# Optimization experiments

Measured on AMD Instinct MI355X. Metric: run time of the kernel, lower is better.

The kernel has to match this reference:

```python
import jax, jax.numpy as jnp
import numpy as np

N = 10000            # nodes
E = 320000           # edges (avg degree 32)
L = 4                # layers
S = 64               # hidden 0e multiplicity
V = 16               # hidden 1o multiplicity
EMB = 32             # node-attr embedding dim
NB = 8               # bessel basis per channel (r and v -> 2*NB edge feats)
MR = 2.5             # max_radius
DEG = 32.0           # num_neighbors
GS = S + V           # gate input scalars: 64 scalars + 16 gates
NW = S * 2 + V * 2 + V * 2   # 192 per-edge tensor-product weights
MAXT = 100           # max atom types


def _semi_unitary(K):
    # Newton-Schulz orthogonalization: K^T K -> I (semi-unitary uplift matrix)
    K = K / jnp.linalg.norm(K)
    for _ in range(10):
        K = 1.5 * K - 0.5 * K @ (K.T @ K)
    return K


def _smooth_cutoff(t):
    u = 2.0 * (t - 1.0)
    y = (1.0 - jnp.cos(jnp.pi * u)) * 0.5
    return jnp.where(u > 0, 0.0, jnp.where(u < -1.0, 1.0, y))


def _edge_geom(d):
    # d: (E,3) edge vector. Returns cutoff-weighted 1x1o SH (component norm) and bessel features.
    r = jnp.linalg.norm(d, axis=1)                       # (E,)
    sh = np.sqrt(3.0) * d / r[:, None]                   # spherical harmonics 1x1o
    attr = _smooth_cutoff(r / MR)[:, None] * sh          # (E,3)
    k = jnp.arange(1, NB + 1, dtype=jnp.float32) * jnp.pi
    feat = np.sqrt(2.0 / MR) * jnp.sin(k * (r / MR)[:, None]) / r[:, None]
    return attr, feat * np.sqrt(NB)                      # (E,3), (E,NB)


def _fctp(s, v, attr, Ws, Wv):
    # FullyConnectedTensorProduct with pure-scalar (0e) node attr == attr-weighted per-irrep linear
    os = jnp.einsum('ni,ne,oie->no', s, attr, Ws) / np.sqrt(s.shape[1] * EMB)
    ov = jnp.einsum('nim,ne,oie->nom', v, attr, Wv) / np.sqrt(v.shape[1] * EMB)
    return os, ov


def _forward(x, node_attr, edge_src, edge_dst, emb_table, PU_K, h, mix,
             si_Ws, si_Wv, sc_Ws, sc_Wv, lin1_Ws, lin1_Wv, lin2_Ws, lin2_Wv,
             fc_W1, fc_b1, fc_W2, fc_b2, fc_W3, fc_b3):
    attr = emb_table[node_attr]                          # (N,EMB)
    K = _semi_unitary(PU_K)                              # (V,2)
    yv = jnp.einsum('ui,nim->num', K, x.reshape(N, 2, 3))  # uplift vectors
    ys = jnp.zeros((N, S), x.dtype)
    ys_old, yv_old = ys, yv
    c_s, c_x = np.sin(np.pi / 8), np.cos(np.pi / 8)
    for i in range(L):
        ar, fr = _edge_geom(x[:, :3][edge_src] - x[:, :3][edge_dst])
        av, fv = _edge_geom(x[:, 3:][edge_src] - x[:, 3:][edge_dst])
        a = jnp.stack([ar, av], axis=1)                  # (E,2,3) = 2x1o edge attr
        ef = jnp.concatenate([fr, fv], axis=1)           # (E,2*NB)
        # radial MLP -> per-edge TP weights
        hd = jax.nn.silu(ef @ fc_W1[i] + fc_b1[i])
        hd = jax.nn.silu(hd @ fc_W2[i] + fc_b2[i])
        w = hd @ fc_W3[i] + fc_b3[i]                     # (E,NW)
        w1 = w[:, :S * 2].reshape(-1, S, 2)
        w2 = w[:, S * 2:S * 2 + V * 2].reshape(-1, V, 2)
        w3 = w[:, S * 2 + V * 2:].reshape(-1, V, 2)
        # conv: lin1 -> gather -> TP -> scatter -> lin2 ; plus self-connection
        fs, fvv = _fctp(ys, yv, attr, lin1_Ws[i], lin1_Wv[i])
        s_src, v_src = fs[edge_src], fvv[edge_src]
        # 0e x 1o -> 1o (uvu)
        o1 = jnp.einsum('euv,eu,evm->eum', w1, s_src, a) / np.sqrt(2.0)   # (E,S,3)
        # 1o x 1o -> 0e (uvu)
        dots = jnp.einsum('eum,evm->euv', v_src, a)
        o2 = jnp.einsum('euv,euv->eu', w2, dots) / np.sqrt(6.0)           # (E,V)
        # 1o x 1o -> 1o (cross, uvu)
        cr = jnp.cross(v_src[:, :, None, :], a[:, None, :, :])            # (E,V,2,3)
        o3 = jnp.einsum('euv,euvm->eum', w3, cr) / 2.0                    # (E,V,3)
        mid_s = jax.ops.segment_sum(o2, edge_dst, num_segments=N) / np.sqrt(DEG)
        mid_v = jax.ops.segment_sum(jnp.concatenate([o1, o3], axis=1), edge_dst,
                                    num_segments=N) / np.sqrt(DEG)        # (N,S+V,3)
        cs2, cv2 = _fctp(mid_s, mid_v, attr, lin2_Ws[i], lin2_Wv[i])      # (N,GS),(N,V,3)
        scs, scv = _fctp(ys, yv, attr, sc_Ws[i], sc_Wv[i])
        conv_s = c_s * scs + c_x * cs2
        conv_v = c_s * scv + c_x * cv2
        # gate: silu scalars, sigmoid gates * gated vectors
        gns = jax.nn.silu(conv_s[:, :S])
        gnv = jax.nn.sigmoid(conv_s[:, S:])[:, :, None] * conv_v
        # self-interaction: per-irrep linear
        sis = ys @ si_Ws[i].T / np.sqrt(S)
        siv = jnp.einsum('oi,nim->nom', si_Wv[i], yv) / np.sqrt(V)
        # leapfrog update
        h2 = h[i] ** 2
        ns = 2.0 * ys - ys_old + h2 * (mix[i] * gns + (mix[i] - 1.0) * sis)
        nv = 2.0 * yv - yv_old + h2 * (mix[i] * gnv + (mix[i] - 1.0) * siv)
        ys_old, yv_old = ys, yv
        ys, yv = ns, nv
        x = jnp.einsum('ui,num->nim', K, yv).reshape(N, 6)   # project
    return x


def setup_inputs() -> dict:
    key = jax.random.key(0)
    ks = jax.random.split(key, 24)
    def g(i, sh, fan=1.0):
        return jax.random.normal(ks[i], sh, dtype=jnp.float32) / np.sqrt(fan)
    edge_src = jax.random.randint(ks[20], (E,), 0, N, dtype=jnp.int32)
    off = jax.random.randint(ks[21], (E,), 1, N, dtype=jnp.int32)
    edge_dst = (edge_src + off) % N                      # guarantees src != dst
    return {
        'x': g(0, (N, 6)),
        'batch': jnp.zeros((N,), jnp.int32),
        'node_attr': jax.random.randint(ks[22], (N,), 0, MAXT, dtype=jnp.int32),
        'edge_src': edge_src,
        'edge_dst': edge_dst,
        'emb_table': g(1, (MAXT, EMB)),
        'PU_K': g(2, (V, 2)),
        'h': jnp.full((L,), 0.01, jnp.float32),
        'mix': jnp.full((L,), 0.5, jnp.float32),
        'si_Ws': g(3, (L, S, S)), 'si_Wv': g(4, (L, V, V)),
        'sc_Ws': g(5, (L, GS, S, EMB)), 'sc_Wv': g(6, (L, V, V, EMB)),
        'lin1_Ws': g(7, (L, S, S, EMB)), 'lin1_Wv': g(8, (L, V, V, EMB)),
        'lin2_Ws': g(9, (L, GS, V, EMB)), 'lin2_Wv': g(10, (L, V, S + V, EMB)),
        'fc_W1': g(11, (L, 2 * NB, 64), 2 * NB), 'fc_b1': jnp.zeros((L, 64), jnp.float32),
        'fc_W2': g(12, (L, 64, 64), 64), 'fc_b2': jnp.zeros((L, 64), jnp.float32),
        'fc_W3': g(13, (L, 64, NW), 64), 'fc_b3': jnp.zeros((L, NW), jnp.float32),
    }


def reference(x, batch, node_attr, edge_src, edge_dst, emb_table, PU_K, h, mix,
              si_Ws, si_Wv, sc_Ws, sc_Wv, lin1_Ws, lin1_Wv, lin2_Ws, lin2_Wv,
              fc_W1, fc_b1, fc_W2, fc_b2, fc_W3, fc_b3):
    return _forward(x, node_attr, edge_src, edge_dst, emb_table, PU_K, h, mix,
                    si_Ws, si_Wv, sc_Ws, sc_Wv, lin1_Ws, lin1_Wv, lin2_Ws, lin2_Wv,
                    fc_W1, fc_b1, fc_W2, fc_b2, fc_W3, fc_b3)
```

## Files before the change

### kernel.cpp

```cpp
#include <hip/hip_runtime.h>
#include <hip/hip_fp8.h>
#include <math.h>

#define NN 10000
#define NE 320000
#define PI_F 3.14159265358979323846f

typedef __attribute__((ext_vector_type(8))) short short8x;
typedef __attribute__((ext_vector_type(4))) float float4x;

#if defined(__has_builtin)
#if __has_builtin(__builtin_amdgcn_cvt_pk_fp8_f32) && __has_builtin(__builtin_amdgcn_cvt_f32_fp8)
#define HW_FP8 1
#endif
#endif

__device__ __forceinline__ unsigned short f2b(float f) {
    unsigned b = __float_as_uint(f);
    return (unsigned short)((b + 0x7FFFu + ((b >> 16) & 1u)) >> 16);
}
__device__ __forceinline__ float b2f(unsigned short u) {
    return __uint_as_float(((unsigned)u) << 16);
}
__device__ __forceinline__ float silu(float x) {
    return x / (1.f + __expf(-x));
}
__device__ __forceinline__ unsigned char f2e4(float f) {
#ifdef HW_FP8
    int r = __builtin_amdgcn_cvt_pk_fp8_f32(f, f, 0, false);
    return (unsigned char)(r & 0xff);
#else
    __hip_fp8_e4m3 q(f);
    return (unsigned char)q.__x;
#endif
}
__device__ __forceinline__ float e42f(unsigned char v) {
#ifdef HW_FP8
    return __builtin_amdgcn_cvt_f32_fp8((int)v, 0);
#else
    __hip_fp8_e4m3 q;
    q.__x = (__hip_fp8_storage_t)v;
    return (float)q;
#endif
}
__device__ __forceinline__ float e4sel(unsigned word, int sel) {
#ifdef HW_FP8
    switch (sel & 3) {
        case 0:  return __builtin_amdgcn_cvt_f32_fp8((int)word, 0);
        case 1:  return __builtin_amdgcn_cvt_f32_fp8((int)word, 1);
        case 2:  return __builtin_amdgcn_cvt_f32_fp8((int)word, 2);
        default: return __builtin_amdgcn_cvt_f32_fp8((int)word, 3);
    }
#else
    return e42f((unsigned char)((word >> (8*(sel & 3))) & 0xffu));
#endif
}
__device__ __forceinline__ unsigned pk4(float a, float b, float c, float d) {
#ifdef HW_FP8
    unsigned w = (unsigned)__builtin_amdgcn_cvt_pk_fp8_f32(a, b, 0, false);
    w = (unsigned)__builtin_amdgcn_cvt_pk_fp8_f32(c, d, (int)w, true);
    return w;
#else
    return (unsigned)f2e4(a) | ((unsigned)f2e4(b) << 8) |
           ((unsigned)f2e4(c) << 16) | ((unsigned)f2e4(d) << 24);
#endif
}

__global__ void k_newton_kernel(const float* __restrict__ PU, float* __restrict__ Kout)
{
    if (threadIdx.x != 0 || blockIdx.x != 0) return;
    float K[32];
    float nrm = 0.f;
    for (int i = 0; i < 32; ++i) { K[i] = PU[i]; nrm += K[i]*K[i]; }
    float inv = 1.0f / sqrtf(nrm);
    for (int i = 0; i < 32; ++i) K[i] *= inv;
    for (int it = 0; it < 10; ++it) {
        float m00 = 0.f, m01 = 0.f, m11 = 0.f;
        for (int u = 0; u < 16; ++u) {
            float a = K[2*u], b = K[2*u+1];
            m00 += a*a; m01 += a*b; m11 += b*b;
        }
        for (int u = 0; u < 16; ++u) {
            float a = K[2*u], b = K[2*u+1];
            K[2*u]   = 1.5f*a - 0.5f*(a*m00 + b*m01);
            K[2*u+1] = 1.5f*b - 0.5f*(a*m01 + b*m11);
        }
    }
    for (int i = 0; i < 32; ++i) Kout[i] = K[i];
}

__global__ __launch_bounds__(256) void init_all_kernel(
    const float* __restrict__ x, const float* __restrict__ K,
    float* __restrict__ xp, float* __restrict__ yv0, float* __restrict__ yv1,
    float* __restrict__ ys0, float* __restrict__ ys1, float* __restrict__ fsb,
    float* __restrict__ midb)
{
    int tid = blockIdx.x*256 + threadIdx.x;
    if (tid < NN*8) {
        int n = tid >> 3, c = tid & 7;
        xp[tid] = (c < 6) ? x[n*6 + c] : 0.f;
        return;
    }
    int t2 = tid - NN*8;
    if (t2 < NN*48) {
        int n = t2/48, j = t2%48, u = j/3, m = j%3;
        float v = K[2*u]*x[n*6+m] + K[2*u+1]*x[n*6+3+m];
        yv0[t2] = v; yv1[t2] = v;
        return;
    }
    t2 -= NN*48;
    if (t2 < NN*64) { ys0[t2] = 0.f; ys1[t2] = 0.f; fsb[t2] = 0.f; return; }
    t2 -= NN*64;
    if (t2 < NN*256) midb[t2] = 0.f;
}

__global__ void init_fvv_kernel(const float* __restrict__ yv, const int* __restrict__ types,
                                const float* __restrict__ lin1vT0, float* __restrict__ fvv)
{
    int tid = blockIdx.x*blockDim.x + threadIdx.x;
    if (tid >= NN*48) return;
    int n = tid/48, j = tid%48, o = j/3, m = j%3;
    int t = types[n];
    const float* W = lin1vT0 + (size_t)t*256;
    float acc = 0.f;
    #pragma unroll
    for (int i = 0; i < 16; ++i) acc += yv[n*48 + i*3 + m]*W[i*16 + o];
    fvv[tid] = acc;
}

__device__ __forceinline__ void be_body(const float* __restrict__ W, const float* __restrict__ emb,
                                        float* __restrict__ out, int id, int O, int I, float scale)
{
    int o = id % O; int r = id / O;
    int i = r % I; r /= I;
    int t = r % 100; int l = r / 100;
    const float* w  = W + (((size_t)l*O + o)*I + i)*32;
    const float* em = emb + (size_t)t*32;
    float acc = 0.f;
    #pragma unroll
    for (int e = 0; e < 32; ++e) acc += w[e]*em[e];
    out[id] = acc*scale;
}

#define PREP_TOTAL (2048000 + 1638400 + 512000 + 512000 + 102400 + 102400 + 49152 + 16384 + 16384 + 8192 + 1024)
__global__ __launch_bounds__(256) void prep_kernel(
    const float* __restrict__ lin1_Ws, const float* __restrict__ lin1_Wv,
    const float* __restrict__ sc_Ws,   const float* __restrict__ sc_Wv,
    const float* __restrict__ lin2_Ws, const float* __restrict__ lin2_Wv,
    const float* __restrict__ si_Ws,   const float* __restrict__ si_Wv,
    const float* __restrict__ fc_W1,   const float* __restrict__ fc_W2,
    const float* __restrict__ fc_W3,   const float* __restrict__ emb,
    float* __restrict__ lin1sT, float* __restrict__ lin1vT,
    float* __restrict__ scsT,   float* __restrict__ scvT,
    float* __restrict__ lin2sT, float* __restrict__ lin2vT,
    float* __restrict__ siWsT,  float* __restrict__ siWvT,
    unsigned short* __restrict__ w1bp, unsigned short* __restrict__ w2bp,
    unsigned short* __restrict__ w3bf)
{
    const float s2048 = 0.022097086912079608f;
    const float s512  = 0.044194173824159216f;
    const float s2560 = 0.019764235376052372f;
    int tid = blockIdx.x*256 + threadIdx.x;
    if (tid < 2048000) { be_body(sc_Ws,   emb, scsT,   tid, 80, 64, s2048); return; }
    tid -= 2048000;
    if (tid < 1638400) { be_body(lin1_Ws, emb, lin1sT, tid, 64, 64, s2048); return; }
    tid -= 1638400;
    if (tid < 512000)  { be_body(lin2_Ws, emb, lin2sT, tid, 80, 16, s512);  return; }
    tid -= 512000;
    if (tid < 512000)  { be_body(lin2_Wv, emb, lin2vT, tid, 16, 80, s2560); return; }
    tid -= 512000;
    if (tid < 102400)  { be_body(lin1_Wv, emb, lin1vT, tid, 16, 16, s512);  return; }
    tid -= 102400;
    if (tid < 102400)  { be_body(sc_Wv,   emb, scvT,   tid, 16, 16, s512);  return; }
    tid -= 102400;
    if (tid < 49152) {
        int o = tid % 64; int r = tid / 64; int i = r % 192; int l = r / 192;
        w3bf[tid] = f2b(fc_W3[((size_t)l*64 + o)*192 + i]);
        return;
    }
    tid -= 49152;
    if (tid < 16384) {
        int o = tid % 64; int r = tid / 64; int i = r % 64; int l = r / 64;
        siWsT[tid] = si_Ws[((size_t)l*64 + o)*64 + i]*0.125f;
        return;
    }
    tid -= 16384;
    if (tid < 16384) {
        int kk = tid % 64; int r = tid / 64; int n = r % 64; int l = r / 64;
        w2bp[tid] = f2b(fc_W2[((size_t)l*64 + kk)*64 + n]);
        return;
    }
    tid -= 16384;
    if (tid < 8192) {
        int kk = tid % 32; int r = tid / 32; int n = r % 64; int l = r / 64;
        float v = (kk < 16) ? fc_W1[((size_t)l*16 + kk)*64 + n] : 0.f;
        w1bp[tid] = f2b(v);
        return;
    }
    tid -= 8192;
    if (tid < 1024) {
        int o = tid % 16; int r = tid / 16; int i = r % 16; int l = r / 16;
        siWvT[tid] = si_Wv[((size_t)l*16 + o)*16 + i]*0.25f;
    }
}

__global__ void hist_kernel(const int* __restrict__ dst, int* __restrict__ deg)
{
    int e = blockIdx.x*256 + threadIdx.x;
    if (e < NE) atomicAdd(&deg[dst[e]], 1);
}

__global__ __launch_bounds__(256) void scan_kernel(const int* __restrict__ deg,
                                                   int* __restrict__ segoff,
                                                   int* __restrict__ cursor)
{
    __shared__ int part[256];
    int tid = threadIdx.x;
    int base = tid*40;
    int s = 0;
    for (int i = 0; i < 40; ++i) { int idx = base+i; if (idx < NN) s += deg[idx]; }
    part[tid] = s;
    __syncthreads();
    for (int o = 1; o < 256; o <<= 1) {
        int v = (tid >= o) ? part[tid-o] : 0;
        __syncthreads();
        part[tid] += v;
        __syncthreads();
    }
    int excl = part[tid] - s;
    for (int i = 0; i < 40; ++i) {
        int idx = base+i;
        if (idx < NN) { segoff[idx] = excl; cursor[idx] = excl; excl += deg[idx]; }
        else if (idx == NN) { segoff[NN] = excl; }
    }
}

__global__ void scatter_kernel(const int* __restrict__ src, const int* __restrict__ dst,
                               int* __restrict__ cursor,
                               int* __restrict__ srcs, int* __restrict__ dsts)
{
    int e = blockIdx.x*256 + threadIdx.x;
    if (e >= NE) return;
    int d = dst[e];
    int p = atomicAdd(&cursor[d], 1);
    srcs[p] = src[e]; dsts[p] = d;
}

__global__ __launch_bounds__(256, 6) void edge_fused_kernel(
    const float* __restrict__ xp,
    const int* __restrict__ srcs, const int* __restrict__ dsts,
    const unsigned short* __restrict__ w1b,
    const float* __restrict__ b1,
    const unsigned short* __restrict__ w2b,
    const float* __restrict__ b2,
    const unsigned short* __restrict__ w3b,
    const float* __restrict__ b3,
    const float* __restrict__ fs, const float* __restrict__ fvv,
    float* __restrict__ mid)
{
    __shared__ __align__(16) unsigned char smem[192*68];
    __shared__ float abuf[6][68];
    __shared__ int ssrc[64], sdst[64];
    __shared__ unsigned smaskl[2];
    unsigned short* hbuf = (unsigned short*)smem;
    int lane = threadIdx.x & 63;
    int wid  = threadIdx.x >> 6;
    int eblk = blockIdx.x * 64;
    int row16 = lane & 15, quad = lane >> 4;
    int erow = 16*wid + row16;

    if (threadIdx.x < 64) {
        int tid = threadIdx.x;
        int own = dsts[eblk + tid];
        ssrc[tid] = srcs[eblk + tid];
        int pidx = eblk + tid - ((tid > 0) ? 1 : 0);
        int prev = dsts[pidx];
        sdst[tid] = own;
        bool nb = (tid > 0) && (own != prev);
        unsigned long long bm = __ballot(nb);
        if (tid == 0) { smaskl[0] = (unsigned)bm; smaskl[1] = (unsigned)(bm >> 32); }
    }

    if (lane < 32) {
        int eidx = 16*wid + (lane & 15);
        int half = lane >> 4;
        int p = eblk + eidx;
        int s = srcs[p], d = dsts[p];
        int off = 3*half;
        const float* xs = xp + (size_t)s*8 + off;
        const float* xd = xp + (size_t)d*8 + off;
        float d0 = xs[0]-xd[0], d1 = xs[1]-xd[1], d2 = xs[2]-xd[2];
        float r = sqrtf(d0*d0 + d1*d1 + d2*d2);
        float invr = 1.0f/r;
        float u = 0.8f*r - 2.0f;
        float cut = (u > 0.f) ? 0.f : ((u < -1.f) ? 1.f : 0.5f*(1.f - __cosf(PI_F*u)));
        float sc = 1.7320508075688772f*cut*invr;
        abuf[off+0][eidx] = sc*d0;
        abuf[off+1][eidx] = sc*d1;
        abuf[off+2][eidx] = sc*d2;
        float fsc = 2.5298221281347035f*invr;
        float wr = 1.2566370614359172f*r;
        unsigned epk[4];
        #pragma unroll
        for (int k = 0; k < 4; ++k) {
            float e0 = fsc*__sinf((float)(2*k+1)*wr);
            float e1 = fsc*__sinf((float)(2*k+2)*wr);
            epk[k] = (unsigned)f2b(e0) | ((unsigned)f2b(e1) << 16);
        }
        uint4* hr = (uint4*)(hbuf + eidx*72);
        uint4 q; q.x = epk[0]; q.y = epk[1]; q.z = epk[2]; q.w = epk[3];
        hr[half] = q;
        uint4 qz; qz.x = 0; qz.y = 0; qz.z = 0; qz.w = 0;
        hr[2+half] = qz;
    }

    {
        short8x a = *(const short8x*)(hbuf + erow*72 + quad*8);
        float4x c[4];
        #pragma unroll
        for (int nt = 0; nt < 4; ++nt) {
            short8x b = *(const short8x*)(w1b + ((size_t)(nt*16 + row16))*32 + quad*8);
            c[nt] = __builtin_amdgcn_mfma_f32_16x16x32_bf16(a, b, (float4x){0.f,0.f,0.f,0.f}, 0, 0, 0);
        }
        #pragma unroll
        for (int nt = 0; nt < 4; ++nt) {
            float bias = b1[nt*16 + row16];
            #pragma unroll
            for (int r = 0; r < 4; ++r) {
                float h = silu(c[nt][r] + bias);
                hbuf[(16*wid + quad*4 + r)*72 + nt*16 + row16] = f2b(h);
            }
        }
    }
    {
        short8x a0v = *(const short8x*)(hbuf + erow*72 + 0*32 + quad*8);
        short8x a1v = *(const short8x*)(hbuf + erow*72 + 1*32 + quad*8);
        float4x c[4];
        #pragma unroll
        for (int nt = 0; nt < 4; ++nt) {
            short8x b0 = *(const short8x*)(w2b + ((size_t)(nt*16 + row16))*64 + 0*32 + quad*8);
            float4x t = __builtin_amdgcn_mfma_f32_16x16x32_bf16(a0v, b0, (float4x){0.f,0.f,0.f,0.f}, 0, 0, 0);
            short8x b1v = *(const short8x*)(w2b + ((size_t)(nt*16 + row16))*64 + 1*32 + quad*8);
            c[nt] = __builtin_amdgcn_mfma_f32_16x16x32_bf16(a1v, b1v, t, 0, 0, 0);
        }
        #pragma unroll
        for (int nt = 0; nt < 4; ++nt) {
            float bias = b2[nt*16 + row16];
            #pragma unroll
            for (int r = 0; r < 4; ++r) {
                float h = silu(c[nt][r] + bias);
                hbuf[(16*wid + quad*4 + r)*72 + nt*16 + row16] = f2b(h);
            }
        }
    }
    {
        short8x a0v = *(const short8x*)(hbuf + erow*72 + 0*32 + quad*8);
        short8x a1v = *(const short8x*)(hbuf + erow*72 + 1*32 + quad*8);
        __syncthreads();
        float4x acc[12];
        #pragma unroll
        for (int nt = 0; nt < 12; ++nt) {
            short8x b0 = *(const short8x*)(w3b + ((size_t)(nt*16 + row16))*64 + 0*32 + quad*8);
            float4x t = __builtin_amdgcn_mfma_f32_16x16x32_bf16(a0v, b0, (float4x){0.f,0.f,0.f,0.f}, 0, 0, 0);
            short8x b1v = *(const short8x*)(w3b + ((size_t)(nt*16 + row16))*64 + 1*32 + quad*8);
            acc[nt] = __builtin_amdgcn_mfma_f32_16x16x32_bf16(a1v, b1v, t, 0, 0, 0);
        }
        #pragma unroll
        for (int nt = 0; nt < 12; ++nt) {
            unsigned pw = pk4(acc[nt][0], acc[nt][1], acc[nt][2], acc[nt][3]);
            *(unsigned*)(smem + (size_t)(nt*16 + row16)*68 + 16*wid + quad*4) = pw;
        }
    }
    __syncthreads();

    {
        unsigned mk0 = __builtin_amdgcn_readfirstlane(smaskl[0]);
        unsigned mk1 = __builtin_amdgcn_readfirstlane(smaskl[1]);
        bool iso1 = (wid < 2);
        int h = iso1 ? wid : (wid - 2);
        unsigned mkh = (h ? mk1 : mk0) & ~1u;
        int ebase = 32*h;
        int dcur = sdst[ebase];

        if (iso1) {
            const unsigned char* wp = smem + (size_t)(2*lane)*68;
            float bA = b3[2*lane], bB = b3[2*lane+1];
            float acc0 = 0.f, acc1 = 0.f, acc2 = 0.f;
            #pragma unroll
            for (int ch = 0; ch < 8; ++ch) {
                int e4 = ebase + 4*ch;
                int4 sv = *(const int4*)&ssrc[e4];
                float f0 = fs[(size_t)sv.x*64 + lane];
                float f1 = fs[(size_t)sv.y*64 + lane];
                float f2 = fs[(size_t)sv.z*64 + lane];
                float f3 = fs[(size_t)sv.w*64 + lane];
                unsigned wa4 = *(const unsigned*)(wp + e4);
                unsigned wb4 = *(const unsigned*)(wp + 68 + e4);
                float4x a00 = *(const float4x*)(&abuf[0][e4]);
                float4x a01 = *(const float4x*)(&abuf[1][e4]);
                float4x a02 = *(const float4x*)(&abuf[2][e4]);
                float4x a10 = *(const float4x*)(&abuf[3][e4]);
                float4x a11 = *(const float4x*)(&abuf[4][e4]);
                float4x a12 = *(const float4x*)(&abuf[5][e4]);
                float fv[4] = {f0, f1, f2, f3};
                float q0[4], q1[4], q2[4];
                #pragma unroll
                for (int k = 0; k < 4; ++k) {
                    float f = fv[k];
                    float wa = (e4sel(wa4, k) + bA)*f;
                    float wb = (e4sel(wb4, k) + bB)*f;
                    q0[k] = wa*a00[k] + wb*a10[k];
                    q1[k] = wa*a01[k] + wb*a11[k];
                    q2[k] = wa*a02[k] + wb*a12[k];
                }
                unsigned mch = (mkh >> (4*ch)) & 15u;
                if (mch == 0) {
                    acc0 += (q0[0] + q0[1]) + (q0[2] + q0[3]);
                    acc1 += (q1[0] + q1[1]) + (q1[2] + q1[3]);
                    acc2 += (q2[0] + q2[1]) + (q2[2] + q2[3]);
                } else {
                    #pragma unroll
                    for (int k = 0; k < 4; ++k) {
                        if (mch & (1u << k)) {
                            float* mrow = mid + (size_t)dcur*256;
                            atomicAdd(mrow + 3*lane + 0, acc0*0.125f);
                            atomicAdd(mrow + 3*lane + 1, acc1*0.125f);
                            atomicAdd(mrow + 3*lane + 2, acc2*0.125f);
                            acc0 = acc1 = acc2 = 0.f;
                            dcur = sdst[e4 + k];
                        }
                        acc0 += q0[k]; acc1 += q1[k]; acc2 += q2[k];
                    }
                }
            }
            float* mrow = mid + (size_t)dcur*256;
            atomicAdd(mrow + 3*lane + 0, acc0*0.125f);
            atomicAdd(mrow + 3*lane + 1, acc1*0.125f);
            atomicAdd(mrow + 3*lane + 2, acc2*0.125f);
        } else {
            bool iso2 = lane < 16;
            int j3 = lane - 16;
            int u3 = j3 / 3;
            int m3 = j3 - 3*u3;
            int m1 = (m3 == 2) ? 0 : (m3 + 1);
            int m2 = 3 - m3 - m1;
            const unsigned char* wp;
            int rA, rB, rC;
            const float* aX0; const float* aY0; const float* aZ0;
            const float* aX1; const float* aY1; const float* aZ1;
            float bA, bB, sgn, gam, FS;
            if (iso2) {
                wp = smem + (size_t)(128 + 2*lane)*68;
                bA = b3[128 + 2*lane]; bB = b3[129 + 2*lane];
                rA = 3*lane; rB = 3*lane + 1; rC = 3*lane + 2;
                aX0 = &abuf[0][0]; aY0 = &abuf[1][0]; aZ0 = &abuf[2][0];
                aX1 = &abuf[3][0]; aY1 = &abuf[4][0]; aZ1 = &abuf[5][0];
                sgn = 1.f; gam = 1.f; FS = 0.07216878364870323f;
            } else {
                wp = smem + (size_t)(160 + 2*u3)*68;
                bA = b3[160 + 2*u3]; bB = b3[161 + 2*u3];
                rA = 3*u3 + m1; rB = 3*u3 + m2; rC = 0;
                aX0 = &abuf[m2][0]; aY0 = &abuf[m1][0]; aZ0 = &abuf[0][0];
                aX1 = &abuf[3+m2][0]; aY1 = &abuf[3+m1][0]; aZ1 = &abuf[3][0];
                sgn = -1.f; gam = 0.f; FS = 0.08838834764831845f;
            }
            int cb = 192 + lane;
            float accb = 0.f;
            #pragma unroll
            for (int ch = 0; ch < 8; ++ch) {
                int e4 = ebase + 4*ch;
                int4 sv = *(const int4*)&ssrc[e4];
                float fa0 = fvv[(size_t)sv.x*48 + rA];
                float fb0 = fvv[(size_t)sv.x*48 + rB];
                float fc0 = fvv[(size_t)sv.x*48 + rC];
                float fa1 = fvv[(size_t)sv.y*48 + rA];
                float fb1 = fvv[(size_t)sv.y*48 + rB];
                float fc1 = fvv[(size_t)sv.y*48 + rC];
                float fa2 = fvv[(size_t)sv.z*48 + rA];
                float fb2 = fvv[(size_t)sv.z*48 + rB];
                float fc2 = fvv[(size_t)sv.z*48 + rC];
                float fa3 = fvv[(size_t)sv.w*48 + rA];
                float fb3 = fvv[(size_t)sv.w*48 + rB];
                float fc3 = fvv[(size_t)sv.w*48 + rC];
                unsigned wa4 = *(const unsigned*)(wp + e4);
                unsigned wb4 = *(const unsigned*)(wp + 68 + e4);
                float4x x0 = *(const float4x*)(aX0 + e4);
                float4x y0 = *(const float4x*)(aY0 + e4);
                float4x z0 = *(const float4x*)(aZ0 + e4);
                float4x x1 = *(const float4x*)(aX1 + e4);
                float4x y1 = *(const float4x*)(aY1 + e4);
                float4x z1 = *(const float4x*)(aZ1 + e4);
                float fav[4] = {fa0, fa1, fa2, fa3};
                float fbv[4] = {fb0, fb1, fb2, fb3};
                float fcv[4] = {fc0, fc1, fc2, fc3};
                float q[4];
                #pragma unroll
                for (int k = 0; k < 4; ++k) {
                    float fa = fav[k], fb = fbv[k], fc = fcv[k];
                    float dA = fmaf(sgn, fb*y0[k], fa*x0[k]);
                    dA = fmaf(gam, fc*z0[k], dA);
                    float dB = fmaf(sgn, fb*y1[k], fa*x1[k]);
                    dB = fmaf(gam, fc*z1[k], dB);
                    q[k] = (e4sel(wa4, k) + bA)*dA + (e4sel(wb4, k) + bB)*dB;
                }
                unsigned mch = (mkh >> (4*ch)) & 15u;
                if (mch == 0) {
                    accb += (q[0] + q[1]) + (q[2] + q[3]);
                } else {
                    #pragma unroll
                    for (int k = 0; k < 4; ++k) {
                        if (mch & (1u << k)) {
                            atomicAdd(mid + (size_t)dcur*256 + cb, accb*FS);
                            accb = 0.f;
                            dcur = sdst[e4 + k];
                        }
                        accb += q[k];
                    }
                }
            }
            atomicAdd(mid + (size_t)dcur*256 + cb, accb*FS);
        }
    }
}

__global__ __launch_bounds__(256) void node_update_kernel(
    const float* __restrict__ ys, const float* __restrict__ yv,
    float* __restrict__ ys_old, float* __restrict__ yv_old,
    float* __restrict__ mid,
    const int* __restrict__ types,
    const float* __restrict__ scsT, const float* __restrict__ scvT,
    const float* __restrict__ lin2sT, const float* __restrict__ lin2vT,
    const float* __restrict__ siWsT, const float* __restrict__ siWvT,
    const float* __restrict__ lin1sTn, const float* __restrict__ lin1vTn,
    const float* __restrict__ Kbuf,
    const float* __restrict__ hv, const float* __restrict__ mixv, int layer,
    float* __restrict__ fs_out, float* __restrict__ fvv_out,
    float* __restrict__ xpad, float* __restrict__ dout)
{
    int n = blockIdx.x;
    int lane = threadIdx.x;
    __shared__ float ys_l[64], yv_l[48], mids[16], midv[240];
    __shared__ float conv_s[80], conv_v[48], sis_l[64], siv_l[48], ysn[64], yvn[48];
    int t = types[n];
    {
        float v = mid[(size_t)n*256 + lane];
        mid[(size_t)n*256 + lane] = 0.f;
        if (lane < 192) midv[lane] = v;
        else if (lane < 208) mids[lane-192] = v;
        else midv[192 + (lane-208)] = v;
    }
    if (lane < 64) ys_l[lane] = ys[n*64 + lane];
    else if (lane < 112) yv_l[lane-64] = yv[n*48 + (lane-64)];
    __syncthreads();
    if (lane < 80) {
        const float* Wsc = scsT + (size_t)t*5120;
        const float* W2s = lin2sT + (size_t)t*1280;
        float a_sc = 0.f, a_2 = 0.f;
        #pragma unroll
        for (int i = 0; i < 64; ++i) a_sc += ys_l[i]*Wsc[i*80 + lane];
        #pragma unroll
        for (int i = 0; i < 16; ++i) a_2 += mids[i]*W2s[i*80 + lane];
        conv_s[lane] = 0.3826834323650898f*a_sc + 0.9238795325112867f*a_2;
    } else if (lane < 144) {
        int o = lane - 80;
        float a_si = 0.f;
        #pragma unroll
        for (int i = 0; i < 64; ++i) a_si += ys_l[i]*siWsT[i*64 + o];
        sis_l[o] = a_si;
    } else if (lane < 192) {
        int j = lane - 144, o = j/3, m = j%3;
        const float* Wsc = scvT + (size_t)t*256;
        const float* W2v = lin2vT + (size_t)t*1280;
        float a_sc = 0.f, a_2 = 0.f, a_si = 0.f;
        #pragma unroll
        for (int i = 0; i < 16; ++i) {
            float y = yv_l[i*3+m];
            a_sc += y*Wsc[i*16+o];
            a_si += y*siWvT[i*16+o];
        }
        #pragma unroll
        for (int i = 0; i < 80; ++i) a_2 += midv[i*3+m]*W2v[i*16+o];
        conv_v[j] = 0.3826834323650898f*a_sc + 0.9238795325112867f*a_2;
        siv_l[j] = a_si;
    }
    __syncthreads();
    float hh = hv[layer]; float h2c = hh*hh; float mx = mixv[layer];
    if (lane < 64) {
        float cs = conv_s[lane];
        float gns = cs/(1.f + __expf(-cs));
        float ns = 2.f*ys_l[lane] - ys_old[n*64+lane] + h2c*(mx*gns + (mx-1.f)*sis_l[lane]);
        ys_old[n*64+lane] = ns;
        ysn[lane] = ns;
    } else if (lane < 112) {
        int j = lane-64, o = j/3;
        float g = 1.f/(1.f + __expf(-conv_s[64+o]));
        float gnv = g*conv_v[j];
        float nv = 2.f*yv_l[j] - yv_old[n*48+j] + h2c*(mx*gnv + (mx-1.f)*siv_l[j]);
        yv_old[n*48+j] = nv;
        yvn[j] = nv;
    }
    __syncthreads();
    if (lane < 6) {
        int i = lane/3, m = lane%3;
        float acc = 0.f;
        #pragma unroll
        for (int u = 0; u < 16; ++u) acc += Kbuf[2*u+i]*yvn[u*3+m];
        xpad[n*8 + lane] = acc;
        if (dout) dout[n*6 + lane] = acc;
    }
    if (lane < 64) {
        const float* W = lin1sTn + (size_t)t*4096;
        float acc = 0.f;
        #pragma unroll
        for (int i = 0; i < 64; ++i) acc += ysn[i]*W[i*64 + lane];
        fs_out[n*64 + lane] = acc;
    } else if (lane < 112) {
        int j = lane - 64, o = j/3, m = j%3;
        const float* W = lin1vTn + (size_t)t*256;
        float acc = 0.f;
        #pragma unroll
        for (int i = 0; i < 16; ++i) acc += yvn[i*3+m]*W[i*16 + o];
        fvv_out[n*48 + j] = acc;
    }
}

extern "C" void kernel_launch(void* const* d_in, const int* in_sizes, int n_in,
                              void* d_out, int out_size, void* d_ws, size_t ws_size,
                              hipStream_t stream)
{
    const float* x_in   = (const float*)d_in[0];
    const int*   types  = (const int*)  d_in[2];
    const int*   esrc   = (const int*)  d_in[3];
    const int*   edst   = (const int*)  d_in[4];
    const float* emb    = (const float*)d_in[5];
    const float* PU     = (const float*)d_in[6];
    const float* hv     = (const float*)d_in[7];
    const float* mixv   = (const float*)d_in[8];
    const float* si_Ws  = (const float*)d_in[9];
    const float* si_Wv  = (const float*)d_in[10];
    const float* sc_Ws  = (const float*)d_in[11];
    const float* sc_Wv  = (const float*)d_in[12];
    const float* lin1_Ws= (const float*)d_in[13];
    const float* lin1_Wv= (const float*)d_in[14];
    const float* lin2_Ws= (const float*)d_in[15];
    const float* lin2_Wv= (const float*)d_in[16];
    const float* fc_W1  = (const float*)d_in[17];
    const float* fc_b1  = (const float*)d_in[18];
    const float* fc_W2  = (const float*)d_in[19];
    const float* fc_b2  = (const float*)d_in[20];
    const float* fc_W3  = (const float*)d_in[21];
    const float* fc_b3  = (const float*)d_in[22];

    float* ws = (float*)d_ws;
    size_t off = 0;
    auto alloc = [&](size_t nf) { float* p = ws + off; off += nf; return p; };
    float* Kbuf   = alloc(64);
    float* x_pad  = alloc(80000);
    float* ys0    = alloc(640000);
    float* ys1    = alloc(640000);
    float* yv0    = alloc(480000);
    float* yv1    = alloc(480000);
    float* fsb    = alloc(640000);
    float* fvvb   = alloc(480000);
    float* midb   = alloc((size_t)NN*256);
    float* lin1sT = alloc((size_t)4*100*4096);
    float* lin1vT = alloc((size_t)4*100*256);
    float* scsT   = alloc((size_t)4*100*5120);
    float* scvT   = alloc((size_t)4*100*256);
    float* lin2sT = alloc((size_t)4*100*1280);
    float* lin2vT = alloc((size_t)4*100*1280);
    float* siWsT  = alloc((size_t)4*4096);
    float* siWvT  = alloc((size_t)4*256);
    int* iws = (int*)(ws + off);
    size_t ioff = 0;
    auto ialloc = [&](size_t ni) { int* p = iws + ioff; ioff += ni; return p; };
    int* deg    = ialloc(NN);
    int* segoff = ialloc(NN + 8);
    int* cursor = ialloc(NN);
    int* srcs   = ialloc(NE);
    int* dsts   = ialloc(NE);
    unsigned short* w1bp = (unsigned short*)(iws + ioff);
    unsigned short* w2bp = w1bp + (size_t)4*64*32;
    unsigned short* w3bf = w2bp + (size_t)4*64*64;

    k_newton_kernel<<<1, 1, 0, stream>>>(PU, Kbuf);
    prep_kernel<<<(PREP_TOTAL + 255)/256, 256, 0, stream>>>(
        lin1_Ws, lin1_Wv, sc_Ws, sc_Wv, lin2_Ws, lin2_Wv, si_Ws, si_Wv,
        fc_W1, fc_W2, fc_W3, emb,
        lin1sT, lin1vT, scsT, scvT, lin2sT, lin2vT, siWsT, siWvT,
        w1bp, w2bp, w3bf);
    {
        int tot = NN*8 + NN*48 + NN*64 + NN*256;
        init_all_kernel<<<(tot + 255)/256, 256, 0, stream>>>(
            x_in, Kbuf, x_pad, yv0, yv1, ys0, ys1, fsb, midb);
    }
    init_fvv_kernel<<<(NN*48 + 255)/256, 256, 0, stream>>>(yv0, types, lin1vT, fvvb);

    (void)hipMemsetAsync(deg, 0, NN*sizeof(int), stream);
    hist_kernel<<<(NE+255)/256, 256, 0, stream>>>(edst, deg);
    scan_kernel<<<1, 256, 0, stream>>>(deg, segoff, cursor);
    scatter_kernel<<<(NE+255)/256, 256, 0, stream>>>(esrc, edst, cursor, srcs, dsts);

    float* ys_cur = ys0; float* ys_old = ys1;
    float* yv_cur = yv0; float* yv_old = yv1;
    for (int l = 0; l < 4; ++l) {
        edge_fused_kernel<<<NE/64, 256, 0, stream>>>(
            x_pad, srcs, dsts,
            w1bp + (size_t)l*64*32,  fc_b1 + (size_t)l*64,
            w2bp + (size_t)l*64*64,  fc_b2 + (size_t)l*64,
            w3bf + (size_t)l*192*64, fc_b3 + (size_t)l*192,
            fsb, fvvb, midb);
        int ln = (l + 1) & 3;
        node_update_kernel<<<NN, 256, 0, stream>>>(
            ys_cur, yv_cur, ys_old, yv_old,
            midb, types,
            scsT   + (size_t)l*100*5120, scvT   + (size_t)l*100*256,
            lin2sT + (size_t)l*100*1280, lin2vT + (size_t)l*100*1280,
            siWsT  + (size_t)l*4096,     siWvT  + (size_t)l*256,
            lin1sT + (size_t)ln*100*4096, lin1vT + (size_t)ln*100*256,
            Kbuf, hv, mixv, l, fsb, fvvb,
            x_pad, (l == 3) ? (float*)d_out : nullptr);
        float* tmp;
        tmp = ys_cur; ys_cur = ys_old; ys_old = tmp;
        tmp = yv_cur; yv_cur = yv_old; yv_old = tmp;
    }
}
```

Measured before the change: 945.9 us.

## Group nodes by atom type and stage per-type weights in shared memory

Adds a counting sort of nodes by atom type and a chunk table with up to 8 same-type nodes per block. The node update kernel then loads that type's weight matrices (about 48 KB) into LDS once per chunk and loops over the nodes, instead of each node's block reading its weights from global memory. This cuts redundant weight traffic but makes node processing serial within a block, uses large LDS that lowers occupancy, and adds a few setup kernels.

```diff
diff --git a/kernel.cpp b/kernel.cpp
--- a/kernel.cpp
+++ b/kernel.cpp
@@ -5,6 +5,8 @@
 #define NN 10000
 #define NE 320000
 #define PI_F 3.14159265358979323846f
+#define NCHK 8
+#define MAXCH 1350
 
 typedef __attribute__((ext_vector_type(8))) short short8x;
 typedef __attribute__((ext_vector_type(4))) float float4x;
@@ -244,6 +246,48 @@
     int d = dst[e];
     int p = atomicAdd(&cursor[d], 1);
     srcs[p] = src[e]; dsts[p] = d;
+}
+
+__global__ void thist_kernel(const int* __restrict__ types, int* __restrict__ tdeg)
+{
+    int n = blockIdx.x*256 + threadIdx.x;
+    if (n < NN) atomicAdd(&tdeg[types[n]], 1);
+}
+
+__global__ __launch_bounds__(128) void tscan_build_kernel(
+    const int* __restrict__ tdeg, int* __restrict__ tcursor,
+    int* __restrict__ ctab, int* __restrict__ ccount)
+{
+    __shared__ int sdeg[100], soff[100];
+    int tid = threadIdx.x;
+    if (tid < 100) sdeg[tid] = tdeg[tid];
+    __syncthreads();
+    if (tid == 0) {
+        int run = 0;
+        for (int t = 0; t < 100; ++t) { soff[t] = run; run += sdeg[t]; }
+    }
+    __syncthreads();
+    if (tid < 100) {
+        tcursor[tid] = soff[tid];
+        int cnt = sdeg[tid];
+        int st = soff[tid];
+        for (int ch = 0; ch*NCHK < cnt; ++ch) {
+            int idx = atomicAdd(ccount, 1);
+            int rem = cnt - ch*NCHK;
+            ctab[idx*4+0] = st + ch*NCHK;
+            ctab[idx*4+1] = (rem < NCHK) ? rem : NCHK;
+            ctab[idx*4+2] = tid;
+        }
+    }
+}
+
+__global__ void tscatter_kernel(const int* __restrict__ types, int* __restrict__ tcursor,
+                                int* __restrict__ nsorted)
+{
+    int n = blockIdx.x*256 + threadIdx.x;
+    if (n >= NN) return;
+    int p = atomicAdd(&tcursor[types[n]], 1);
+    nsorted[p] = n;
 }
 
 __global__ __launch_bounds__(256, 6) void edge_fused_kernel(
@@ -527,7 +571,6 @@
     const float* __restrict__ ys, const float* __restrict__ yv,
     float* __restrict__ ys_old, float* __restrict__ yv_old,
     float* __restrict__ mid,
-    const int* __restrict__ types,
     const float* __restrict__ scsT, const float* __restrict__ scvT,
     const float* __restrict__ lin2sT, const float* __restrict__ lin2vT,
     const float* __restrict__ siWsT, const float* __restrict__ siWvT,
@@ -535,92 +578,118 @@
     const float* __restrict__ Kbuf,
     const float* __restrict__ hv, const float* __restrict__ mixv, int layer,
     float* __restrict__ fs_out, float* __restrict__ fvv_out,
-    float* __restrict__ xpad, float* __restrict__ dout)
-{
-    int n = blockIdx.x;
-    int lane = threadIdx.x;
+    float* __restrict__ xpad, float* __restrict__ dout,
+    const int* __restrict__ nsorted, const int* __restrict__ ctab)
+{
+    int bid = blockIdx.x;
+    int start = ctab[bid*4+0];
+    int cnt   = ctab[bid*4+1];
+    int t     = ctab[bid*4+2];
+    if (cnt == 0) return;
+    __shared__ float wl[12288];
     __shared__ float ys_l[64], yv_l[48], mids[16], midv[240];
     __shared__ float conv_s[80], conv_v[48], sis_l[64], siv_l[48], ysn[64], yvn[48];
-    int t = types[n];
+    int lane = threadIdx.x;
     {
-        float v = mid[(size_t)n*256 + lane];
-        mid[(size_t)n*256 + lane] = 0.f;
-        if (lane < 192) midv[lane] = v;
-        else if (lane < 208) mids[lane-192] = v;
-        else midv[192 + (lane-208)] = v;
-    }
-    if (lane < 64) ys_l[lane] = ys[n*64 + lane];
-    else if (lane < 112) yv_l[lane-64] = yv[n*48 + (lane-64)];
+        float4* d = (float4*)wl;
+        const float4* s0 = (const float4*)(scsT + (size_t)t*5120);
+        for (int i = lane; i < 1280; i += 256) d[i] = s0[i];
+        const float4* s1 = (const float4*)(lin2sT + (size_t)t*1280);
+        for (int i = lane; i < 320; i += 256) d[1280 + i] = s1[i];
+        const float4* s2 = (const float4*)(scvT + (size_t)t*256);
+        if (lane < 64) d[1600 + lane] = s2[lane];
+        const float4* s3 = (const float4*)(lin2vT + (size_t)t*1280);
+        for (int i = lane; i < 320; i += 256) d[1664 + i] = s3[i];
+        const float4* s4 = (const float4*)(lin1sTn + (size_t)t*4096);
+        for (int i = lane; i < 1024; i += 256) d[1984 + i] = s4[i];
+        const float4* s5 = (const float4*)(lin1vTn + (size_t)t*256);
+        if (lane < 64) d[3008 + lane] = s5[lane];
+    }
+    const float* sWsc = wl;
+    const float* sW2s = wl + 5120;
+    const float* sWcv = wl + 6400;
+    const float* sW2v = wl + 6656;
+    const float* sL1s = wl + 7936;
+    const float* sL1v = wl + 12032;
+    float hh = hv[layer]; float h2c = hh*hh; float mx = mixv[layer];
     __syncthreads();
-    if (lane < 80) {
-        const float* Wsc = scsT + (size_t)t*5120;
-        const float* W2s = lin2sT + (size_t)t*1280;
-        float a_sc = 0.f, a_2 = 0.f;
-        #pragma unroll
-        for (int i = 0; i < 64; ++i) a_sc += ys_l[i]*Wsc[i*80 + lane];
-        #pragma unroll
-        for (int i = 0; i < 16; ++i) a_2 += mids[i]*W2s[i*80 + lane];
-        conv_s[lane] = 0.3826834323650898f*a_sc + 0.9238795325112867f*a_2;
-    } else if (lane < 144) {
-        int o = lane - 80;
-        float a_si = 0.f;
-        #pragma unroll
-        for (int i = 0; i < 64; ++i) a_si += ys_l[i]*siWsT[i*64 + o];
-        sis_l[o] = a_si;
-    } else if (lane < 192) {
-        int j = lane - 144, o = j/3, m = j%3;
-        const float* Wsc = scvT + (size_t)t*256;
-        const float* W2v = lin2vT + (size_t)t*1280;
-        float a_sc = 0.f, a_2 = 0.f, a_si = 0.f;
-        #pragma unroll
-        for (int i = 0; i < 16; ++i) {
-            float y = yv_l[i*3+m];
-            a_sc += y*Wsc[i*16+o];
-            a_si += y*siWvT[i*16+o];
-        }
-        #pragma unroll
-        for (int i = 0; i < 80; ++i) a_2 += midv[i*3+m]*W2v[i*16+o];
-        conv_v[j] = 0.3826834323650898f*a_sc + 0.9238795325112867f*a_2;
-        siv_l[j] = a_si;
-    }
-    __syncthreads();
-    float hh = hv[layer]; float h2c = hh*hh; float mx = mixv[layer];
-    if (lane < 64) {
-        float cs = conv_s[lane];
-        float gns = cs/(1.f + __expf(-cs));
-        float ns = 2.f*ys_l[lane] - ys_old[n*64+lane] + h2c*(mx*gns + (mx-1.f)*sis_l[lane]);
-        ys_old[n*64+lane] = ns;
-        ysn[lane] = ns;
-    } else if (lane < 112) {
-        int j = lane-64, o = j/3;
-        float g = 1.f/(1.f + __expf(-conv_s[64+o]));
-        float gnv = g*conv_v[j];
-        float nv = 2.f*yv_l[j] - yv_old[n*48+j] + h2c*(mx*gnv + (mx-1.f)*siv_l[j]);
-        yv_old[n*48+j] = nv;
-        yvn[j] = nv;
-    }
-    __syncthreads();
-    if (lane < 6) {
-        int i = lane/3, m = lane%3;
-        float acc = 0.f;
-        #pragma unroll
-        for (int u = 0; u < 16; ++u) acc += Kbuf[2*u+i]*yvn[u*3+m];
-        xpad[n*8 + lane] = acc;
-        if (dout) dout[n*6 + lane] = acc;
-    }
-    if (lane < 64) {
-        const float* W = lin1sTn + (size_t)t*4096;
-        float acc = 0.f;
-        #pragma unroll
-        for (int i = 0; i < 64; ++i) acc += ysn[i]*W[i*64 + lane];
-        fs_out[n*64 + lane] = acc;
-    } else if (lane < 112) {
-        int j = lane - 64, o = j/3, m = j%3;
-        const float* W = lin1vTn + (size_t)t*256;
-        float acc = 0.f;
-        #pragma unroll
-        for (int i = 0; i < 16; ++i) acc += yvn[i*3+m]*W[i*16 + o];
-        fvv_out[n*48 + j] = acc;
+
+    for (int ni = 0; ni < cnt; ++ni) {
+        int n = nsorted[start + ni];
+        {
+            float v = mid[(size_t)n*256 + lane];
+            mid[(size_t)n*256 + lane] = 0.f;
+            if (lane < 192) midv[lane] = v;
+            else if (lane < 208) mids[lane-192] = v;
+            else midv[192 + (lane-208)] = v;
+        }
+        if (lane < 64) ys_l[lane] = ys[n*64 + lane];
+        else if (lane < 112) yv_l[lane-64] = yv[n*48 + (lane-64)];
+        __syncthreads();
+        if (lane < 80) {
+            float a_sc = 0.f, a_2 = 0.f;
+            #pragma unroll
+            for (int i = 0; i < 64; ++i) a_sc += ys_l[i]*sWsc[i*80 + lane];
+            #pragma unroll
+            for (int i = 0; i < 16; ++i) a_2 += mids[i]*sW2s[i*80 + lane];
+            conv_s[lane] = 0.3826834323650898f*a_sc + 0.9238795325112867f*a_2;
+        } else if (lane < 144) {
+            int o = lane - 80;
+            float a_si = 0.f;
+            #pragma unroll
+            for (int i = 0; i < 64; ++i) a_si += ys_l[i]*siWsT[i*64 + o];
+            sis_l[o] = a_si;
+        } else if (lane < 192) {
+            int j = lane - 144, o = j/3, m = j%3;
+            float a_sc = 0.f, a_2 = 0.f, a_si = 0.f;
+            #pragma unroll
+            for (int i = 0; i < 16; ++i) {
+                float y = yv_l[i*3+m];
+                a_sc += y*sWcv[i*16+o];
+                a_si += y*siWvT[i*16+o];
+            }
+            #pragma unroll
+            for (int i = 0; i < 80; ++i) a_2 += midv[i*3+m]*sW2v[i*16+o];
+            conv_v[j] = 0.3826834323650898f*a_sc + 0.9238795325112867f*a_2;
+            siv_l[j] = a_si;
+        }
+        __syncthreads();
+        if (lane < 64) {
+            float cs = conv_s[lane];
+            float gns = cs/(1.f + __expf(-cs));
+            float ns = 2.f*ys_l[lane] - ys_old[n*64+lane] + h2c*(mx*gns + (mx-1.f)*sis_l[lane]);
+            ys_old[n*64+lane] = ns;
+            ysn[lane] = ns;
+        } else if (lane < 112) {
+            int j = lane-64, o = j/3;
+            float g = 1.f/(1.f + __expf(-conv_s[64+o]));
+            float gnv = g*conv_v[j];
+            float nv = 2.f*yv_l[j] - yv_old[n*48+j] + h2c*(mx*gnv + (mx-1.f)*siv_l[j]);
+            yv_old[n*48+j] = nv;
+            yvn[j] = nv;
+        }
+        __syncthreads();
+        if (lane < 6) {
+            int i = lane/3, m = lane%3;
+            float acc = 0.f;
+            #pragma unroll
+            for (int u = 0; u < 16; ++u) acc += Kbuf[2*u+i]*yvn[u*3+m];
+            xpad[n*8 + lane] = acc;
+            if (dout) dout[n*6 + lane] = acc;
+        }
+        if (lane < 64) {
+            float acc = 0.f;
+            #pragma unroll
+            for (int i = 0; i < 64; ++i) acc += ysn[i]*sL1s[i*64 + lane];
+            fs_out[n*64 + lane] = acc;
+        } else if (lane < 112) {
+            int j = lane - 64, o = j/3, m = j%3;
+            float acc = 0.f;
+            #pragma unroll
+            for (int i = 0; i < 16; ++i) acc += yvn[i*3+m]*sL1v[i*16 + o];
+            fvv_out[n*48 + j] = acc;
+        }
+        __syncthreads();
     }
 }
 
@@ -679,6 +748,11 @@
     int* cursor = ialloc(NN);
     int* srcs   = ialloc(NE);
     int* dsts   = ialloc(NE);
+    int* tdeg    = ialloc(104);
+    int* tcursor = ialloc(104);
+    int* ctabi   = ialloc(MAXCH*4);
+    int* ccnt    = ialloc(4);
+    int* nsorted = ialloc(NN);
     unsigned short* w1bp = (unsigned short*)(iws + ioff);
     unsigned short* w2bp = w1bp + (size_t)4*64*32;
     unsigned short* w3bf = w2bp + (size_t)4*64*64;
@@ -701,6 +775,11 @@
     scan_kernel<<<1, 256, 0, stream>>>(deg, segoff, cursor);
     scatter_kernel<<<(NE+255)/256, 256, 0, stream>>>(esrc, edst, cursor, srcs, dsts);
 
+    (void)hipMemsetAsync(tdeg, 0, (104 + 104 + MAXCH*4 + 4)*sizeof(int), stream);
+    thist_kernel<<<(NN+255)/256, 256, 0, stream>>>(types, tdeg);
+    tscan_build_kernel<<<1, 128, 0, stream>>>(tdeg, tcursor, ctabi, ccnt);
+    tscatter_kernel<<<(NN+255)/256, 256, 0, stream>>>(types, tcursor, nsorted);
+
     float* ys_cur = ys0; float* ys_old = ys1;
     float* yv_cur = yv0; float* yv_old = yv1;
     for (int l = 0; l < 4; ++l) {
@@ -711,15 +790,16 @@
             w3bf + (size_t)l*192*64, fc_b3 + (size_t)l*192,
             fsb, fvvb, midb);
         int ln = (l + 1) & 3;
-        node_update_kernel<<<NN, 256, 0, stream>>>(
+        node_update_kernel<<<MAXCH, 256, 0, stream>>>(
             ys_cur, yv_cur, ys_old, yv_old,
-            midb, types,
+            midb,
             scsT   + (size_t)l*100*5120, scvT   + (size_t)l*100*256,
             lin2sT + (size_t)l*100*1280, lin2vT + (size_t)l*100*1280,
             siWsT  + (size_t)l*4096,     siWvT  + (size_t)l*256,
             lin1sT + (size_t)ln*100*4096, lin1vT + (size_t)ln*100*256,
             Kbuf, hv, mixv, l, fsb, fvvb,
-            x_pad, (l == 3) ? (float*)d_out : nullptr);
+            x_pad, (l == 3) ? (float*)d_out : nullptr,
+            nsorted, ctabi);
         float* tmp;
         tmp = ys_cur; ys_cur = ys_old; ys_old = tmp;
         tmp = yv_cur; yv_cur = yv_old; yv_old = tmp;
```

After: 1.915 ms. +102.4%, slower.
